# Kernel optimization log

Hardware: AMD Instinct MI355X
Metric: run time of the kernel (lower is better)

The kernel has to match this reference:

```python
import jax, jax.numpy as jnp
import numpy as np

KERNEL = 3
STRIDE = 1
PAD = 1


def setup_inputs() -> dict:
    key = jax.random.key(0)
    k1, k2 = jax.random.split(key)
    x = jax.random.normal(k1, (16, 32, 512, 512), dtype=jnp.float32)
    # original init: torch.rand(O, I, k, k) / (k*k)
    kernels = jax.random.uniform(k2, (32, 32, KERNEL, KERNEL), dtype=jnp.float32) / (KERNEL * KERNEL)
    return {"x": x, "kernels": kernels}


def reference(x, kernels):
    # Equivalent math to the unfold+einsum im2col conv2d: pad, extract kxk
    # windows with stride, contract over (in_channels, kh, kw).
    # Expressed as a direct convolution (cross-correlation), which is the
    # same computation without materializing the 6D window tensor.
    out = jax.lax.conv_general_dilated(
        x, kernels,
        window_strides=(STRIDE, STRIDE),
        padding=((PAD, PAD), (PAD, PAD)),
        dimension_numbers=("NCHW", "OIHW", "NCHW"),
    )
    return out  # [B, out_channels, H_out, W_out]
```

## Files before the change

### kernel.cpp

```cpp
#include <hip/hip_runtime.h>
#include <hip/hip_bf16.h>

typedef __attribute__((ext_vector_type(8))) short bf16x8;
typedef __attribute__((ext_vector_type(4))) float f32x4;
typedef __attribute__((ext_vector_type(4))) unsigned int u32x4;

#define NC 32
#define NO 32
#define HH 512
#define WWD 512
#define HW (HH * WWD)

#define TH 8
#define TW 64
#define HALO_H (TH + 2)
#define HALO_W (TW + 2)
#define NPIX (HALO_H * HALO_W)
#define NUNIT (NPIX * 4)
#define NITER 16

#define WS_STRIDE 289

__device__ __forceinline__ unsigned short f2bf(float f) {
    unsigned u = __builtin_bit_cast(unsigned, f);
    u += 0x7FFFu + ((u >> 16) & 1u);
    return (unsigned short)(u >> 16);
}

__global__ __launch_bounds__(512, 2)
void conv3x3_mfma(const float* __restrict__ x,
                  const float* __restrict__ wk,
                  float* __restrict__ out) {
    __shared__ __align__(16) char smem[NPIX * 64];

    const int tid   = threadIdx.x;
    const int lane  = tid & 63;
    const int wv    = tid >> 6;
    const int col16 = lane & 15;
    const int g4    = lane >> 4;

    const int w0    = blockIdx.x * TW;
    const int hbase = blockIdx.y * (TH * NITER);
    const int b     = blockIdx.z;

    float* ws = (float*)smem;
    for (int i = tid; i < NO * 288; i += 512) {
        int oc = i / 288;
        ws[oc * WS_STRIDE + (i - oc * 288)] = wk[i];
    }
    __syncthreads();

    bf16x8 wf[9][2];
    #pragma unroll
    for (int tap = 0; tap < 9; ++tap) {
        #pragma unroll
        for (int n = 0; n < 2; ++n) {
            bf16x8 f;
            #pragma unroll
            for (int j = 0; j < 8; ++j) {
                float v = ws[(n * 16 + col16) * WS_STRIDE + (g4 * 8 + j) * 9 + tap];
                f[j] = (short)f2bf(v);
            }
            wf[tap][n] = f;
        }
    }

    const float* xb = x + (size_t)b * NC * HW;
    float* ob = out + (size_t)b * NO * HW;

    float sv[6][8];

    auto load_tile = [&](int h0) {
        #pragma unroll
        for (int k = 0; k < 6; ++k) {
            int u = tid + k * 512;
            if (u < NUNIT) {
                int g  = u / NPIX;
                int p  = u - g * NPIX;
                int hh = p / HALO_W;
                int ww = p - hh * HALO_W;
                int row = h0 + hh - 1;
                int cl  = w0 + ww - 1;
                bool ok = ((unsigned)row < (unsigned)HH) && ((unsigned)cl < (unsigned)WWD);
                const float* src = xb + (g * 8) * HW + row * WWD + cl;
                #pragma unroll
                for (int j = 0; j < 8; ++j) {
                    float t = 0.f;
                    if (ok) t = src[j * HW];
                    sv[k][j] = t;
                }
            }
        }
    };

    load_tile(hbase);

    for (int it = 0; it < NITER; ++it) {
        const int h0 = hbase + it * TH;

        __syncthreads();

        #pragma unroll
        for (int k = 0; k < 6; ++k) {
            int u = tid + k * 512;
            if (u < NUNIT) {
                int g = u / NPIX;
                int p = u - g * NPIX;
                unsigned q0 = (unsigned)f2bf(sv[k][0]) | ((unsigned)f2bf(sv[k][1]) << 16);
                unsigned q1 = (unsigned)f2bf(sv[k][2]) | ((unsigned)f2bf(sv[k][3]) << 16);
                unsigned q2 = (unsigned)f2bf(sv[k][4]) | ((unsigned)f2bf(sv[k][5]) << 16);
                unsigned q3 = (unsigned)f2bf(sv[k][6]) | ((unsigned)f2bf(sv[k][7]) << 16);
                int byte = (p * 64 + g * 16) ^ ((p & 7) << 4);
                u32x4 q = { q0, q1, q2, q3 };
                *(u32x4*)(smem + byte) = q;
            }
        }

        if (it + 1 < NITER) load_tile(h0 + TH);

        __syncthreads();

        f32x4 acc[4][2];
        #pragma unroll
        for (int m = 0; m < 4; ++m) {
            #pragma unroll
            for (int n = 0; n < 2; ++n) {
                f32x4 z = {0.f, 0.f, 0.f, 0.f};
                acc[m][n] = z;
            }
        }

        #pragma unroll
        for (int dh = 0; dh < 3; ++dh) {
            #pragma unroll
            for (int dw = 0; dw < 3; ++dw) {
                const int tap = dh * 3 + dw;
                #pragma unroll
                for (int m = 0; m < 4; ++m) {
                    int p = (wv + dh) * HALO_W + m * 16 + col16 + dw;
                    int byte = (p * 64 + g4 * 16) ^ ((p & 7) << 4);
                    bf16x8 a = *(bf16x8*)(smem + byte);
                    acc[m][0] = __builtin_amdgcn_mfma_f32_16x16x32_bf16(a, wf[tap][0], acc[m][0], 0, 0, 0);
                    acc[m][1] = __builtin_amdgcn_mfma_f32_16x16x32_bf16(a, wf[tap][1], acc[m][1], 0, 0, 0);
                }
            }
        }

        float* orow = ob + (h0 + wv) * WWD + w0;
        #pragma unroll
        for (int m = 0; m < 4; ++m) {
            #pragma unroll
            for (int n = 0; n < 2; ++n) {
                int oc = n * 16 + col16;
                int wc = m * 16 + g4 * 4;
                *(f32x4*)(orow + oc * HW + wc) = acc[m][n];
            }
        }
    }
}

extern "C" void kernel_launch(void* const* d_in, const int* in_sizes, int n_in,
                              void* d_out, int out_size, void* d_ws, size_t ws_size,
                              hipStream_t stream) {
    const float* x  = (const float*)d_in[0];
    const float* wk = (const float*)d_in[1];
    float* out = (float*)d_out;
    dim3 grid(WWD / TW, HH / (TH * NITER), 16);
    conv3x3_mfma<<<grid, 512, 0, stream>>>(x, wk, out);
}
```

Baseline: 306.6 us.

## Reuse halo rows via ring buffer, keep weights in LDS, raise occupancy

Turns the per-block input tile into a 10-row circular buffer, so each iteration loads only 8 new rows instead of reloading the full 10-row halo. Weights are converted to bf16 once and kept in LDS, then read per tap instead of held in 18 vector registers. This frees registers so launch bounds can ask for 4 blocks per CU. Output stores become nontemporal. The cost is extra LDS reads of weights per tap, a larger LDS footprint, and more complex ring-index arithmetic.

```diff
diff --git a/kernel.cpp b/kernel.cpp
--- a/kernel.cpp
+++ b/kernel.cpp
@@ -6,20 +6,19 @@
 typedef __attribute__((ext_vector_type(4))) unsigned int u32x4;
 
 #define NC 32
-#define NO 32
 #define HH 512
 #define WWD 512
 #define HW (HH * WWD)
 
 #define TH 8
 #define TW 64
-#define HALO_H (TH + 2)
-#define HALO_W (TW + 2)
-#define NPIX (HALO_H * HALO_W)
-#define NUNIT (NPIX * 4)
+#define HALO_W 66
+#define ROWS 10
 #define NITER 16
-
-#define WS_STRIDE 289
+#define XBYTES (ROWS * HALO_W * 64)
+#define WOFF XBYTES
+#define NU8  (8 * HALO_W * 4)
+#define NU10 (ROWS * HALO_W * 4)
 
 __device__ __forceinline__ unsigned short f2bf(float f) {
     unsigned u = __builtin_bit_cast(unsigned, f);
@@ -27,11 +26,15 @@
     return (unsigned short)(u >> 16);
 }
 
-__global__ __launch_bounds__(512, 2)
+__device__ __forceinline__ int xbyte(int p, int g) {
+    return (p * 64 + g * 16) ^ ((p & 7) << 4);
+}
+
+__global__ __launch_bounds__(512, 4)
 void conv3x3_mfma(const float* __restrict__ x,
                   const float* __restrict__ wk,
                   float* __restrict__ out) {
-    __shared__ __align__(16) char smem[NPIX * 64];
+    __shared__ __align__(16) char smem[XBYTES + 9 * 32 * 32 * 2];
 
     const int tid   = threadIdx.x;
     const int lane  = tid & 63;
@@ -43,119 +46,177 @@
     const int hbase = blockIdx.y * (TH * NITER);
     const int b     = blockIdx.z;
 
-    float* ws = (float*)smem;
-    for (int i = tid; i < NO * 288; i += 512) {
-        int oc = i / 288;
-        ws[oc * WS_STRIDE + (i - oc * 288)] = wk[i];
-    }
+    const float* xb = x + (size_t)b * NC * HW;
+    float* ob = out + (size_t)b * NC * HW;
+
+    float sv[6][8];
+
+    #pragma unroll
+    for (int k = 0; k < 6; ++k) {
+        int u = tid + k * 512;
+        if (u < NU10) {
+            int g  = u / (ROWS * HALO_W);
+            int p  = u - g * (ROWS * HALO_W);
+            int hh = p / HALO_W;
+            int ww = p - hh * HALO_W;
+            int row = hbase + hh - 1;
+            int cl  = w0 + ww - 1;
+            bool ok = ((unsigned)row < (unsigned)HH) && ((unsigned)cl < (unsigned)WWD);
+            const float* src = xb + (g * 8) * HW + row * WWD + cl;
+            #pragma unroll
+            for (int j = 0; j < 8; ++j) {
+                float t = 0.f;
+                if (ok) t = src[j * HW];
+                sv[k][j] = t;
+            }
+        }
+    }
+
+    {
+        unsigned short* wl = (unsigned short*)(smem + WOFF);
+        for (int i = tid; i < 9216; i += 512) {
+            int oc = i / 288; int rem = i - oc * 288;
+            int ic = rem / 9; int tap = rem - ic * 9;
+            wl[(tap * 32 + oc) * 32 + ic] = f2bf(wk[i]);
+        }
+    }
+
+    #pragma unroll
+    for (int k = 0; k < 6; ++k) {
+        int u = tid + k * 512;
+        if (u < NU10) {
+            int g = u / (ROWS * HALO_W);
+            int p = u - g * (ROWS * HALO_W);
+            unsigned q0 = (unsigned)f2bf(sv[k][0]) | ((unsigned)f2bf(sv[k][1]) << 16);
+            unsigned q1 = (unsigned)f2bf(sv[k][2]) | ((unsigned)f2bf(sv[k][3]) << 16);
+            unsigned q2 = (unsigned)f2bf(sv[k][4]) | ((unsigned)f2bf(sv[k][5]) << 16);
+            unsigned q3 = (unsigned)f2bf(sv[k][6]) | ((unsigned)f2bf(sv[k][7]) << 16);
+            u32x4 q = { q0, q1, q2, q3 };
+            *(u32x4*)(smem + xbyte(p, g)) = q;
+        }
+    }
+
+    #pragma unroll
+    for (int k = 0; k < 5; ++k) {
+        int u = tid + k * 512;
+        if (u < NU8) {
+            int g  = u / (8 * HALO_W);
+            int p  = u - g * (8 * HALO_W);
+            int hh = p / HALO_W;
+            int ww = p - hh * HALO_W;
+            int row = hbase + 9 + hh;
+            int cl  = w0 + ww - 1;
+            bool ok = ((unsigned)row < (unsigned)HH) && ((unsigned)cl < (unsigned)WWD);
+            const float* src = xb + (g * 8) * HW + row * WWD + cl;
+            #pragma unroll
+            for (int j = 0; j < 8; ++j) {
+                float t = 0.f;
+                if (ok) t = src[j * HW];
+                sv[k][j] = t;
+            }
+        }
+    }
+
     __syncthreads();
 
-    bf16x8 wf[9][2];
-    #pragma unroll
-    for (int tap = 0; tap < 9; ++tap) {
-        #pragma unroll
-        for (int n = 0; n < 2; ++n) {
-            bf16x8 f;
-            #pragma unroll
-            for (int j = 0; j < 8; ++j) {
-                float v = ws[(n * 16 + col16) * WS_STRIDE + (g4 * 8 + j) * 9 + tap];
-                f[j] = (short)f2bf(v);
-            }
-            wf[tap][n] = f;
-        }
-    }
-
-    const float* xb = x + (size_t)b * NC * HW;
-    float* ob = out + (size_t)b * NO * HW;
-
-    float sv[6][8];
-
-    auto load_tile = [&](int h0) {
-        #pragma unroll
-        for (int k = 0; k < 6; ++k) {
-            int u = tid + k * 512;
-            if (u < NUNIT) {
-                int g  = u / NPIX;
-                int p  = u - g * NPIX;
-                int hh = p / HALO_W;
-                int ww = p - hh * HALO_W;
-                int row = h0 + hh - 1;
-                int cl  = w0 + ww - 1;
-                bool ok = ((unsigned)row < (unsigned)HH) && ((unsigned)cl < (unsigned)WWD);
-                const float* src = xb + (g * 8) * HW + row * WWD + cl;
-                #pragma unroll
-                for (int j = 0; j < 8; ++j) {
-                    float t = 0.f;
-                    if (ok) t = src[j * HW];
-                    sv[k][j] = t;
-                }
-            }
-        }
-    };
-
-    load_tile(hbase);
+    int srbase = wv;
+    int wb = 0;
 
     for (int it = 0; it < NITER; ++it) {
-        const int h0 = hbase + it * TH;
-
-        __syncthreads();
-
-        #pragma unroll
-        for (int k = 0; k < 6; ++k) {
-            int u = tid + k * 512;
-            if (u < NUNIT) {
-                int g = u / NPIX;
-                int p = u - g * NPIX;
-                unsigned q0 = (unsigned)f2bf(sv[k][0]) | ((unsigned)f2bf(sv[k][1]) << 16);
-                unsigned q1 = (unsigned)f2bf(sv[k][2]) | ((unsigned)f2bf(sv[k][3]) << 16);
-                unsigned q2 = (unsigned)f2bf(sv[k][4]) | ((unsigned)f2bf(sv[k][5]) << 16);
-                unsigned q3 = (unsigned)f2bf(sv[k][6]) | ((unsigned)f2bf(sv[k][7]) << 16);
-                int byte = (p * 64 + g * 16) ^ ((p & 7) << 4);
-                u32x4 q = { q0, q1, q2, q3 };
-                *(u32x4*)(smem + byte) = q;
-            }
-        }
-
-        if (it + 1 < NITER) load_tile(h0 + TH);
-
-        __syncthreads();
-
         f32x4 acc[4][2];
         #pragma unroll
         for (int m = 0; m < 4; ++m) {
-            #pragma unroll
-            for (int n = 0; n < 2; ++n) {
-                f32x4 z = {0.f, 0.f, 0.f, 0.f};
-                acc[m][n] = z;
-            }
-        }
-
+            f32x4 z = {0.f, 0.f, 0.f, 0.f};
+            acc[m][0] = z; acc[m][1] = z;
+        }
+
+        int rs[3];
         #pragma unroll
         for (int dh = 0; dh < 3; ++dh) {
+            int s = srbase + dh; if (s >= ROWS) s -= ROWS;
+            rs[dh] = s * HALO_W;
+        }
+
+        const char* wls = smem + WOFF;
+        #pragma unroll
+        for (int dh = 0; dh < 3; ++dh) {
             #pragma unroll
             for (int dw = 0; dw < 3; ++dw) {
                 const int tap = dh * 3 + dw;
+                bf16x8 b0 = *(const bf16x8*)(wls + (tap * 32 + col16) * 64 + g4 * 16);
+                bf16x8 b1 = *(const bf16x8*)(wls + (tap * 32 + 16 + col16) * 64 + g4 * 16);
                 #pragma unroll
                 for (int m = 0; m < 4; ++m) {
-                    int p = (wv + dh) * HALO_W + m * 16 + col16 + dw;
-                    int byte = (p * 64 + g4 * 16) ^ ((p & 7) << 4);
-                    bf16x8 a = *(bf16x8*)(smem + byte);
-                    acc[m][0] = __builtin_amdgcn_mfma_f32_16x16x32_bf16(a, wf[tap][0], acc[m][0], 0, 0, 0);
-                    acc[m][1] = __builtin_amdgcn_mfma_f32_16x16x32_bf16(a, wf[tap][1], acc[m][1], 0, 0, 0);
-                }
-            }
-        }
-
-        float* orow = ob + (h0 + wv) * WWD + w0;
-        #pragma unroll
-        for (int m = 0; m < 4; ++m) {
-            #pragma unroll
-            for (int n = 0; n < 2; ++n) {
-                int oc = n * 16 + col16;
-                int wc = m * 16 + g4 * 4;
-                *(f32x4*)(orow + oc * HW + wc) = acc[m][n];
-            }
-        }
+                    int p = rs[dh] + m * 16 + col16 + dw;
+                    bf16x8 a = *(const bf16x8*)(smem + xbyte(p, g4));
+                    acc[m][0] = __builtin_amdgcn_mfma_f32_16x16x32_bf16(a, b0, acc[m][0], 0, 0, 0);
+                    acc[m][1] = __builtin_amdgcn_mfma_f32_16x16x32_bf16(a, b1, acc[m][1], 0, 0, 0);
+                }
+            }
+        }
+
+        {
+            float* orow = ob + (size_t)(hbase + it * 8 + wv) * WWD + w0;
+            #pragma unroll
+            for (int m = 0; m < 4; ++m) {
+                #pragma unroll
+                for (int n = 0; n < 2; ++n) {
+                    float* pp = orow + (size_t)(n * 16 + col16) * HW + m * 16 + g4 * 4;
+                    __builtin_nontemporal_store(acc[m][n], (f32x4*)pp);
+                }
+            }
+        }
+
+        if (it < NITER - 1) {
+            __syncthreads();
+
+            #pragma unroll
+            for (int k = 0; k < 5; ++k) {
+                int u = tid + k * 512;
+                if (u < NU8) {
+                    int g  = u / (8 * HALO_W);
+                    int p  = u - g * (8 * HALO_W);
+                    int hh = p / HALO_W;
+                    int ww = p - hh * HALO_W;
+                    int slot = wb + hh; if (slot >= ROWS) slot -= ROWS;
+                    int pp = slot * HALO_W + ww;
+                    unsigned q0 = (unsigned)f2bf(sv[k][0]) | ((unsigned)f2bf(sv[k][1]) << 16);
+                    unsigned q1 = (unsigned)f2bf(sv[k][2]) | ((unsigned)f2bf(sv[k][3]) << 16);
+                    unsigned q2 = (unsigned)f2bf(sv[k][4]) | ((unsigned)f2bf(sv[k][5]) << 16);
+                    unsigned q3 = (unsigned)f2bf(sv[k][6]) | ((unsigned)f2bf(sv[k][7]) << 16);
+                    u32x4 q = { q0, q1, q2, q3 };
+                    *(u32x4*)(smem + xbyte(pp, g)) = q;
+                }
+            }
+            wb += 8; if (wb >= ROWS) wb -= ROWS;
+
+            if (it < NITER - 2) {
+                #pragma unroll
+                for (int k = 0; k < 5; ++k) {
+                    int u = tid + k * 512;
+                    if (u < NU8) {
+                        int g  = u / (8 * HALO_W);
+                        int p  = u - g * (8 * HALO_W);
+                        int hh = p / HALO_W;
+                        int ww = p - hh * HALO_W;
+                        int row = hbase + 8 * it + 17 + hh;
+                        int cl  = w0 + ww - 1;
+                        bool ok = ((unsigned)row < (unsigned)HH) && ((unsigned)cl < (unsigned)WWD);
+                        const float* src = xb + (g * 8) * HW + row * WWD + cl;
+                        #pragma unroll
+                        for (int j = 0; j < 8; ++j) {
+                            float t = 0.f;
+                            if (ok) t = src[j * HW];
+                            sv[k][j] = t;
+                        }
+                    }
+                }
+            }
+
+            __syncthreads();
+        }
+
+        srbase += 8; if (srbase >= ROWS) srbase -= ROWS;
     }
 }
 
```

Result: slower. 343.8 us (+12.2%).

## Use ring-buffered halo rows with two-deep register prefetch and one barrier per step

Applied to the files above, without the earlier changes.

Turns the shared-memory tile into an 18-row ring buffer. Each iteration now loads only the 8 new input rows and reuses the 2-row halo, where before the full 10-row halo tile was reloaded every time. The loads are double-buffered in registers, with explicit vmcnt waits and sched barriers so global loads overlap the MFMA work, and only one barrier is needed per step. It also drops the XOR swizzle in favour of a channel-group-major LDS layout, and clamps addresses so the loads can be issued unconditionally. The risks are higher register pressure, hand-counted vmcnt values that could be wrong, and possible LDS bank conflicts without the swizzle.

```diff
diff --git a/kernel.cpp b/kernel.cpp
--- a/kernel.cpp
+++ b/kernel.cpp
@@ -5,21 +5,15 @@
 typedef __attribute__((ext_vector_type(4))) float f32x4;
 typedef __attribute__((ext_vector_type(4))) unsigned int u32x4;
 
-#define NC 32
-#define NO 32
 #define HH 512
 #define WWD 512
 #define HW (HH * WWD)
-
-#define TH 8
 #define TW 64
-#define HALO_H (TH + 2)
-#define HALO_W (TW + 2)
-#define NPIX (HALO_H * HALO_W)
-#define NUNIT (NPIX * 4)
+#define HALO_W 66
+#define ROWS 18
+#define NPIX (ROWS * HALO_W)
+#define XBYTES (NPIX * 64)
 #define NITER 16
-
-#define WS_STRIDE 289
 
 __device__ __forceinline__ unsigned short f2bf(float f) {
     unsigned u = __builtin_bit_cast(unsigned, f);
@@ -27,11 +21,108 @@
     return (unsigned short)(u >> 16);
 }
 
+__device__ __forceinline__ void issue8(const float* __restrict__ xb, int row0, int w0,
+                                       float (&sv)[5][8]) {
+    #pragma unroll
+    for (int k = 0; k < 5; ++k) {
+        int u = threadIdx.x + k * 512;
+        int g = u / 640, r = u - g * 640, hh = r / 80, ww = r - hh * 80;
+        int wwc = ww < 66 ? ww : 65;
+        int row = row0 + hh, cl = w0 + wwc - 1;
+        bool ok = (ww < 66) & ((unsigned)row < 512u) & ((unsigned)cl < 512u);
+        int rowc = row < 0 ? 0 : (row > 511 ? 511 : row);
+        int clc  = cl  < 0 ? 0 : (cl  > 511 ? 511 : cl);
+        const float* src = xb + (size_t)(g * 8) * HW + rowc * WWD + clc;
+        #pragma unroll
+        for (int j = 0; j < 8; ++j) { float v = src[(size_t)j * HW]; sv[k][j] = ok ? v : 0.f; }
+    }
+}
+
+__device__ __forceinline__ void write8(char* smem, int wsb, float (&sv)[5][8]) {
+    #pragma unroll
+    for (int k = 0; k < 5; ++k) {
+        int u = threadIdx.x + k * 512;
+        int g = u / 640, r = u - g * 640, hh = r / 80, ww = r - hh * 80;
+        int slot = wsb + hh; if (slot >= ROWS) slot -= ROWS;
+        int p = slot * HALO_W + (ww < 66 ? ww : 0);
+        int byte = (ww < 66) ? (g * NPIX + p) * 16 : XBYTES;
+        unsigned q0 = (unsigned)f2bf(sv[k][0]) | ((unsigned)f2bf(sv[k][1]) << 16);
+        unsigned q1 = (unsigned)f2bf(sv[k][2]) | ((unsigned)f2bf(sv[k][3]) << 16);
+        unsigned q2 = (unsigned)f2bf(sv[k][4]) | ((unsigned)f2bf(sv[k][5]) << 16);
+        unsigned q3 = (unsigned)f2bf(sv[k][6]) | ((unsigned)f2bf(sv[k][7]) << 16);
+        u32x4 q = { q0, q1, q2, q3 };
+        *(u32x4*)(smem + byte) = q;
+    }
+}
+
+template<int WAITN, bool ISS, bool WR, bool BAR>
+__device__ __forceinline__ void conv_body(char* smem, const float* __restrict__ xb,
+                                          float* __restrict__ ob,
+                                          bf16x8 (&wf)[9][2],
+                                          float (&cur)[5][8], float (&nxt)[5][8],
+                                          int srb, int row0, int issrow, int w0,
+                                          int wv, int col16, int g4) {
+    if (ISS) {
+        issue8(xb, issrow, w0, nxt);
+        __builtin_amdgcn_sched_barrier(0);
+    }
+    if constexpr (WAITN == 40)      asm volatile("s_waitcnt vmcnt(40)" ::: "memory");
+    else if constexpr (WAITN == 48) asm volatile("s_waitcnt vmcnt(48)" ::: "memory");
+    else if constexpr (WAITN == 8)  asm volatile("s_waitcnt vmcnt(8)"  ::: "memory");
+    else                            asm volatile("s_waitcnt vmcnt(63)" ::: "memory");
+
+    if (WR) {
+        int wsb = srb + 10; if (wsb >= ROWS) wsb -= ROWS;
+        write8(smem, wsb, cur);
+    }
+
+    f32x4 acc[4][2];
+    #pragma unroll
+    for (int m = 0; m < 4; ++m) {
+        f32x4 z = {0.f, 0.f, 0.f, 0.f};
+        acc[m][0] = z; acc[m][1] = z;
+    }
+    int rs[3];
+    #pragma unroll
+    for (int dh = 0; dh < 3; ++dh) {
+        int s = srb + wv + dh; if (s >= ROWS) s -= ROWS;
+        rs[dh] = s * HALO_W;
+    }
+    const char* xg = smem + g4 * (NPIX * 16);
+    #pragma unroll
+    for (int dh = 0; dh < 3; ++dh) {
+        #pragma unroll
+        for (int dw = 0; dw < 3; ++dw) {
+            const int tap = dh * 3 + dw;
+            #pragma unroll
+            for (int m = 0; m < 4; ++m) {
+                bf16x8 a = *(const bf16x8*)(xg + (rs[dh] + m * 16 + col16 + dw) * 16);
+                acc[m][0] = __builtin_amdgcn_mfma_f32_16x16x32_bf16(a, wf[tap][0], acc[m][0], 0, 0, 0);
+                acc[m][1] = __builtin_amdgcn_mfma_f32_16x16x32_bf16(a, wf[tap][1], acc[m][1], 0, 0, 0);
+            }
+        }
+    }
+    {
+        float* orow = ob + (size_t)(row0 + wv) * WWD + w0;
+        #pragma unroll
+        for (int m = 0; m < 4; ++m)
+            #pragma unroll
+            for (int n = 0; n < 2; ++n)
+                *(f32x4*)(orow + (size_t)(n * 16 + col16) * HW + m * 16 + g4 * 4) = acc[m][n];
+    }
+    if (BAR) {
+        asm volatile("s_waitcnt lgkmcnt(0)" ::: "memory");
+        __builtin_amdgcn_sched_barrier(0);
+        __builtin_amdgcn_s_barrier();
+        __builtin_amdgcn_sched_barrier(0);
+    }
+}
+
 __global__ __launch_bounds__(512, 2)
 void conv3x3_mfma(const float* __restrict__ x,
                   const float* __restrict__ wk,
                   float* __restrict__ out) {
-    __shared__ __align__(16) char smem[NPIX * 64];
+    __shared__ __align__(16) char smem[XBYTES + 16];
 
     const int tid   = threadIdx.x;
     const int lane  = tid & 63;
@@ -40,123 +131,91 @@
     const int g4    = lane >> 4;
 
     const int w0    = blockIdx.x * TW;
-    const int hbase = blockIdx.y * (TH * NITER);
+    const int hbase = blockIdx.y * (8 * NITER);
     const int b     = blockIdx.z;
 
-    float* ws = (float*)smem;
-    for (int i = tid; i < NO * 288; i += 512) {
-        int oc = i / 288;
-        ws[oc * WS_STRIDE + (i - oc * 288)] = wk[i];
-    }
-    __syncthreads();
+    const float* xb = x + (size_t)b * 32 * HW;
+    float* ob = out + (size_t)b * 32 * HW;
 
     bf16x8 wf[9][2];
-    #pragma unroll
-    for (int tap = 0; tap < 9; ++tap) {
-        #pragma unroll
-        for (int n = 0; n < 2; ++n) {
-            bf16x8 f;
+    {
+        float* ws = (float*)smem;
+        for (int i = tid; i < 9216; i += 512) {
+            int oc = i / 288;
+            ws[oc * 289 + (i - oc * 288)] = wk[i];
+        }
+        __syncthreads();
+        #pragma unroll
+        for (int tap = 0; tap < 9; ++tap) {
             #pragma unroll
-            for (int j = 0; j < 8; ++j) {
-                float v = ws[(n * 16 + col16) * WS_STRIDE + (g4 * 8 + j) * 9 + tap];
-                f[j] = (short)f2bf(v);
-            }
-            wf[tap][n] = f;
-        }
-    }
-
-    const float* xb = x + (size_t)b * NC * HW;
-    float* ob = out + (size_t)b * NO * HW;
-
-    float sv[6][8];
-
-    auto load_tile = [&](int h0) {
+            for (int n = 0; n < 2; ++n) {
+                bf16x8 f;
+                #pragma unroll
+                for (int j = 0; j < 8; ++j)
+                    f[j] = (short)f2bf(ws[(n * 16 + col16) * 289 + (g4 * 8 + j) * 9 + tap]);
+                wf[tap][n] = f;
+            }
+        }
+        __syncthreads();
+    }
+
+    {
+        float svp[6][8];
         #pragma unroll
         for (int k = 0; k < 6; ++k) {
             int u = tid + k * 512;
-            if (u < NUNIT) {
-                int g  = u / NPIX;
-                int p  = u - g * NPIX;
-                int hh = p / HALO_W;
-                int ww = p - hh * HALO_W;
-                int row = h0 + hh - 1;
-                int cl  = w0 + ww - 1;
-                bool ok = ((unsigned)row < (unsigned)HH) && ((unsigned)cl < (unsigned)WWD);
-                const float* src = xb + (g * 8) * HW + row * WWD + cl;
+            if (u < 2640) {
+                int g = u / 660, r = u - g * 660, hh = r / 66, ww = r - hh * 66;
+                int row = hbase + hh - 1, cl = w0 + ww - 1;
+                bool ok = ((unsigned)row < 512u) & ((unsigned)cl < 512u);
+                int rowc = row < 0 ? 0 : (row > 511 ? 511 : row);
+                int clc  = cl  < 0 ? 0 : (cl  > 511 ? 511 : cl);
+                const float* src = xb + (size_t)(g * 8) * HW + rowc * WWD + clc;
                 #pragma unroll
-                for (int j = 0; j < 8; ++j) {
-                    float t = 0.f;
-                    if (ok) t = src[j * HW];
-                    sv[k][j] = t;
-                }
-            }
-        }
-    };
-
-    load_tile(hbase);
-
-    for (int it = 0; it < NITER; ++it) {
-        const int h0 = hbase + it * TH;
-
-        __syncthreads();
-
+                for (int j = 0; j < 8; ++j) { float v = src[(size_t)j * HW]; svp[k][j] = ok ? v : 0.f; }
+            }
+        }
         #pragma unroll
         for (int k = 0; k < 6; ++k) {
             int u = tid + k * 512;
-            if (u < NUNIT) {
-                int g = u / NPIX;
-                int p = u - g * NPIX;
-                unsigned q0 = (unsigned)f2bf(sv[k][0]) | ((unsigned)f2bf(sv[k][1]) << 16);
-                unsigned q1 = (unsigned)f2bf(sv[k][2]) | ((unsigned)f2bf(sv[k][3]) << 16);
-                unsigned q2 = (unsigned)f2bf(sv[k][4]) | ((unsigned)f2bf(sv[k][5]) << 16);
-                unsigned q3 = (unsigned)f2bf(sv[k][6]) | ((unsigned)f2bf(sv[k][7]) << 16);
-                int byte = (p * 64 + g * 16) ^ ((p & 7) << 4);
+            if (u < 2640) {
+                int g = u / 660, p = u - g * 660;
+                unsigned q0 = (unsigned)f2bf(svp[k][0]) | ((unsigned)f2bf(svp[k][1]) << 16);
+                unsigned q1 = (unsigned)f2bf(svp[k][2]) | ((unsigned)f2bf(svp[k][3]) << 16);
+                unsigned q2 = (unsigned)f2bf(svp[k][4]) | ((unsigned)f2bf(svp[k][5]) << 16);
+                unsigned q3 = (unsigned)f2bf(svp[k][6]) | ((unsigned)f2bf(svp[k][7]) << 16);
                 u32x4 q = { q0, q1, q2, q3 };
-                *(u32x4*)(smem + byte) = q;
-            }
-        }
-
-        if (it + 1 < NITER) load_tile(h0 + TH);
-
-        __syncthreads();
-
-        f32x4 acc[4][2];
-        #pragma unroll
-        for (int m = 0; m < 4; ++m) {
-            #pragma unroll
-            for (int n = 0; n < 2; ++n) {
-                f32x4 z = {0.f, 0.f, 0.f, 0.f};
-                acc[m][n] = z;
-            }
-        }
-
-        #pragma unroll
-        for (int dh = 0; dh < 3; ++dh) {
-            #pragma unroll
-            for (int dw = 0; dw < 3; ++dw) {
-                const int tap = dh * 3 + dw;
-                #pragma unroll
-                for (int m = 0; m < 4; ++m) {
-                    int p = (wv + dh) * HALO_W + m * 16 + col16 + dw;
-                    int byte = (p * 64 + g4 * 16) ^ ((p & 7) << 4);
-                    bf16x8 a = *(bf16x8*)(smem + byte);
-                    acc[m][0] = __builtin_amdgcn_mfma_f32_16x16x32_bf16(a, wf[tap][0], acc[m][0], 0, 0, 0);
-                    acc[m][1] = __builtin_amdgcn_mfma_f32_16x16x32_bf16(a, wf[tap][1], acc[m][1], 0, 0, 0);
-                }
-            }
-        }
-
-        float* orow = ob + (h0 + wv) * WWD + w0;
-        #pragma unroll
-        for (int m = 0; m < 4; ++m) {
-            #pragma unroll
-            for (int n = 0; n < 2; ++n) {
-                int oc = n * 16 + col16;
-                int wc = m * 16 + g4 * 4;
-                *(f32x4*)(orow + oc * HW + wc) = acc[m][n];
-            }
-        }
-    }
+                *(u32x4*)(smem + (g * NPIX + p) * 16) = q;
+            }
+        }
+    }
+
+    float svA[5][8], svB[5][8];
+    issue8(xb, hbase + 9, w0, svA);
+    __builtin_amdgcn_sched_barrier(0);
+    __syncthreads();
+
+    int srb = 0;
+    conv_body<40, 1, 1, 1>(smem, xb, ob, wf, svA, svB, srb, hbase, hbase + 17, w0, wv, col16, g4);
+    srb = 8;
+    #pragma unroll 1
+    for (int tp = 0; tp < 6; ++tp) {
+        int t1 = 1 + 2 * tp;
+        conv_body<48, 1, 1, 1>(smem, xb, ob, wf, svB, svA, srb,
+                               hbase + 8 * t1, hbase + 8 * t1 + 17, w0, wv, col16, g4);
+        srb += 8; if (srb >= ROWS) srb -= ROWS;
+        conv_body<48, 1, 1, 1>(smem, xb, ob, wf, svA, svB, srb,
+                               hbase + 8 * (t1 + 1), hbase + 8 * (t1 + 1) + 17, w0, wv, col16, g4);
+        srb += 8; if (srb >= ROWS) srb -= ROWS;
+    }
+    conv_body<48, 1, 1, 1>(smem, xb, ob, wf, svB, svA, srb,
+                           hbase + 104, hbase + 121, w0, wv, col16, g4);
+    srb += 8; if (srb >= ROWS) srb -= ROWS;
+    conv_body<8, 0, 1, 1>(smem, xb, ob, wf, svA, svB, srb,
+                          hbase + 112, 0, w0, wv, col16, g4);
+    srb += 8; if (srb >= ROWS) srb -= ROWS;
+    conv_body<63, 0, 0, 0>(smem, xb, ob, wf, svB, svA, srb,
+                           hbase + 120, 0, w0, wv, col16, g4);
 }
 
 extern "C" void kernel_launch(void* const* d_in, const int* in_sizes, int n_in,
@@ -165,6 +224,6 @@
     const float* x  = (const float*)d_in[0];
     const float* wk = (const float*)d_in[1];
     float* out = (float*)d_out;
-    dim3 grid(WWD / TW, HH / (TH * NITER), 16);
+    dim3 grid(WWD / TW, HH / (8 * NITER), 16);
     conv3x3_mfma<<<grid, 512, 0, stream>>>(x, wk, out);
 }
```

After: 313.9 us. 2.4% more time.
